# Kernel tuning notes

Measured on AMD Instinct MI355X. Metric: run time of the kernel, lower is better.

Reference implementation:

```python
import jax, jax.numpy as jnp
import numpy as np

NUM_HEADS = 8
CHUNK = 64          # dialtion / chunck_size
EPS = 1e-5          # InstanceNorm1d eps
NEG = -1e9


def setup_inputs() -> dict:
    key = jax.random.key(0)
    ks = jax.random.split(key, 8)
    N, C, T = 4, 512, 4096
    x = jax.random.normal(ks[0], (N, C, T), dtype=jnp.float32)
    q = jax.random.normal(ks[1], (N, C, T), dtype=jnp.float32)
    k = jax.random.normal(ks[2], (N, C, T), dtype=jnp.float32)
    v = jax.random.normal(ks[3], (N, C, T), dtype=jnp.float32)
    masks = jnp.ones((N, 1, T), dtype=jnp.float32)
    s = 1.0 / np.sqrt(C)
    W_in = jax.random.normal(ks[4], (3 * C, C), dtype=jnp.float32) * s   # packed q/k/v in-proj
    b_in = jnp.zeros((3 * C,), dtype=jnp.float32)
    W_out = jax.random.normal(ks[5], (C, C), dtype=jnp.float32) * s     # out-proj
    b_out = jnp.zeros((C,), dtype=jnp.float32)
    return {"x": x, "q": q, "k": k, "v": v, "masks": masks,
            "W_in": W_in, "b_in": b_in, "W_out": W_out, "b_out": b_out}


def _chunk_attn(q, k, v, masks, W_in, b_in, W_out, b_out):
    # q,k,v: [N, C, T]; masks: [N, 1, T]
    N, C, T = q.shape
    H, Dh = NUM_HEADS, C // NUM_HEADS
    nc = T // CHUNK
    Wq, Wk, Wv = jnp.split(W_in, 3, axis=0)
    bq, bk, bv = jnp.split(b_in, 3, axis=0)

    def proj(t, W, b):
        # [N,C,T] -> chunked heads [N, nc, CHUNK, H, Dh]
        t = t.transpose(0, 2, 1) @ W.T + b            # [N, T, C]
        return t.reshape(N, nc, CHUNK, H, Dh)

    qh = proj(q, Wq, bq)
    kh = proj(k, Wk, bk)
    vh = proj(v, Wv, bv)

    scale = 1.0 / jnp.sqrt(jnp.asarray(Dh, q.dtype))
    # intra-chunk scores: [N, nc, H, CHUNK, CHUNK]
    scores = jnp.einsum('bnqhd,bnkhd->bnhqk', qh, kh) * scale
    km = masks[:, 0, :].reshape(N, nc, CHUNK)         # key validity per chunk
    scores = scores + jnp.where(km[:, :, None, None, :] > 0, 0.0, NEG)
    attn = jax.nn.softmax(scores, axis=-1)
    out = jnp.einsum('bnhqk,bnkhd->bnqhd', attn, vh).reshape(N, T, C)
    out = out @ W_out.T + b_out                        # [N, T, C]
    out = out.transpose(0, 2, 1) * masks               # [N, C, T], re-mask
    return out


def reference(x, q, k, v, masks, W_in, b_in, W_out, b_out):
    out = _chunk_attn(q, k, v, masks, W_in, b_in, W_out, b_out) + x
    # InstanceNorm1d (affine=False): normalize each (n, c) row over T
    mu = jnp.mean(out, axis=2, keepdims=True)
    var = jnp.mean(jnp.square(out - mu), axis=2, keepdims=True)
    return (out - mu) * jax.lax.rsqrt(var + EPS)
```

## Files before the change

### kernel.cpp

```cpp
#include <hip/hip_runtime.h>
#include <hip/hip_bf16.h>

#define NB 4
#define CC 512
#define TT 4096
#define C3 1536
#define CQK 1024
#define NTC (NB*TT*CC)

typedef __attribute__((ext_vector_type(4))) float f32x4;
typedef __attribute__((ext_vector_type(8))) short short8;
typedef unsigned short ushort;
typedef __attribute__((ext_vector_type(8))) ushort u16x8;

__device__ __forceinline__ ushort f2bf(float f){
    union { float f; unsigned u; } x; x.f = f;
    unsigned r = x.u + 0x7fffu + ((x.u >> 16) & 1u);
    return (ushort)(r >> 16);
}

__device__ __forceinline__ ushort2 pk2bf(float a, float b){
    float2 f2; f2.x = a; f2.y = b;
    __hip_bfloat162 h = __float22bfloat162_rn(f2);
    union { __hip_bfloat162 h2; ushort2 u2; } u; u.h2 = h;
    return u.u2;
}

__device__ __forceinline__ void gload16(const void* g, void* l){
    __builtin_amdgcn_global_load_lds((const __attribute__((address_space(1))) void*)g,
                                     (__attribute__((address_space(3))) void*)l,
                                     16, 0, 0);
}

__device__ __forceinline__ int apos(int m, int cb){
    return (m*8 + ((cb + m + (m >> 3)) & 7))*8;
}

__global__ __launch_bounds__(256) void wcvt(const float* __restrict__ Wi,
                                            const float* __restrict__ Wo,
                                            ushort* __restrict__ Wb,
                                            ushort* __restrict__ Wob){
    int idx0 = blockIdx.x * 1024 + threadIdx.x;
    for (int i = 0; i < 4; ++i){
        int idx = idx0 + i*256;
        const float* src; ushort* dst; int j;
        if (idx < 196608){ src = Wi; dst = Wb;  j = idx; }
        else             { src = Wo; dst = Wob; j = idx - 196608; }
        f32x4 vv = *((const f32x4*)src + j);
        ushort4 o;
        *(ushort2*)&o.x = pk2bf(vv[0], vv[1]);
        *(ushort2*)&o.z = pk2bf(vv[2], vv[3]);
        *((ushort4*)dst + j) = o;
    }
}

__global__ __launch_bounds__(256, 3) void proj_gemm(const float* __restrict__ q,
                                                    const float* __restrict__ k,
                                                    const float* __restrict__ v,
                                                    const ushort* __restrict__ Wb,
                                                    const float* __restrict__ b_in,
                                                    ushort* __restrict__ P,
                                                    ushort* __restrict__ Vt){
    __shared__ __align__(16) ushort smem[24576];
    ushort* sA  = smem;
    ushort* sB0 = smem + 8192;
    ushort* sB1 = smem + 16384;
    const int tid = threadIdx.x;
    const int bid = blockIdx.x;
    const int l = (bid & 7)*192 + (bid >> 3);
    const int cotile = l % 12;
    const int mtile  = l / 12;
    const int co0 = cotile * 128;
    const int m0  = mtile * 128;
    const int which = co0 >> 9;
    const float* src = (which == 0) ? q : (which == 1) ? k : v;
    const int n  = m0 >> 12, t0 = m0 & 4095;
    const ushort* Bbase = Wb + (size_t)co0*CC;
    const int w = tid >> 6, lane = tid & 63;
    const int wr = w >> 1, wc = w & 1;
    const int l15 = lane & 15, quad = lane >> 4;
    const int hlf = lane >> 5, tq = lane & 31;

    const int mrB = tid >> 3;
    const int kkB = (tid & 7) ^ (mrB & 7);
    const ushort* gB0 = Bbase + (size_t)mrB*CC + kkB*8;
    const int lB0 = (tid & ~63) * 8;

    const float* Ab = src + (size_t)n*CC*TT + t0 + tq*4;
    const int ce0 = w*16 + hlf*2;

    f32x4 a0[4], a1[4];
    #pragma unroll
    for (int u = 0; u < 4; ++u){
        a0[u] = *(const f32x4*)(Ab + (size_t)(ce0 + u*4    )*TT);
        a1[u] = *(const f32x4*)(Ab + (size_t)(ce0 + u*4 + 1)*TT);
    }
    #pragma unroll
    for (int i = 0; i < 4; ++i)
        gload16(gB0 + (size_t)i*32*CC, sB0 + lB0 + i*2048);
    #pragma unroll
    for (int u = 0; u < 4; ++u){
        int ce = ce0 + u*4;
        int cb = ce >> 3, off = ce & 7;
        #pragma unroll
        for (int j = 0; j < 4; ++j)
            *(ushort2*)&sA[apos(tq*4 + j, cb) + off] = pk2bf(a0[u][j], a1[u][j]);
    }
    __syncthreads();

    f32x4 acc[4][4] = {};
    for (int kb = 0; kb < 8; ++kb){
        ushort* sBc = (kb & 1) ? sB1 : sB0;
        ushort* sBn = (kb & 1) ? sB0 : sB1;
        if (kb < 7){
            const float* Abn = Ab + (size_t)((kb+1)*64)*TT;
            #pragma unroll
            for (int u = 0; u < 4; ++u){
                a0[u] = *(const f32x4*)(Abn + (size_t)(ce0 + u*4    )*TT);
                a1[u] = *(const f32x4*)(Abn + (size_t)(ce0 + u*4 + 1)*TT);
            }
            #pragma unroll
            for (int i = 0; i < 4; ++i)
                gload16(gB0 + (size_t)i*32*CC + (kb+1)*64, sBn + lB0 + i*2048);
        }
        #pragma unroll
        for (int ks = 0; ks < 2; ++ks){
            short8 aF[4], bF[4];
            #pragma unroll
            for (int mi = 0; mi < 4; ++mi){
                int m = wr*64 + mi*16 + l15;
                aF[mi] = *(const short8*)&sA[apos(m, ks*4 + quad)];
            }
            #pragma unroll
            for (int ni = 0; ni < 4; ++ni){
                int m = wc*64 + ni*16 + l15;
                bF[ni] = *(const short8*)&sBc[(m*8 + ((ks*4 + quad) ^ (m & 7)))*8];
            }
            #pragma unroll
            for (int mi = 0; mi < 4; ++mi)
                #pragma unroll
                for (int ni = 0; ni < 4; ++ni)
                    acc[mi][ni] = __builtin_amdgcn_mfma_f32_16x16x32_bf16(
                        aF[mi], bF[ni], acc[mi][ni], 0, 0, 0);
        }
        __syncthreads();
        if (kb < 7){
            #pragma unroll
            for (int u = 0; u < 4; ++u){
                int ce = ce0 + u*4;
                int cb = ce >> 3, off = ce & 7;
                #pragma unroll
                for (int j = 0; j < 4; ++j)
                    *(ushort2*)&sA[apos(tq*4 + j, cb) + off] = pk2bf(a0[u][j], a1[u][j]);
            }
        }
        __syncthreads();
    }

    float bj[4];
    for (int ni = 0; ni < 4; ++ni) bj[ni] = b_in[co0 + wc*64 + ni*16 + l15];

    __syncthreads();
    ushort* sOut = smem;
    if (which < 2){
        for (int mi = 0; mi < 4; ++mi){
            int mrow = wr*64 + mi*16 + quad*4;
            for (int ni = 0; ni < 4; ++ni){
                int col = wc*64 + ni*16 + l15;
                for (int r = 0; r < 4; ++r)
                    sOut[(mrow + r)*136 + col] = f2bf(acc[mi][ni][r] + bj[ni]);
            }
        }
    } else {
        for (int mi = 0; mi < 4; ++mi){
            int mrow = wr*64 + mi*16 + quad*4;
            for (int ni = 0; ni < 4; ++ni){
                int col = wc*64 + ni*16 + l15;
                ushort4 o4;
                o4.x = f2bf(acc[mi][ni][0] + bj[ni]);
                o4.y = f2bf(acc[mi][ni][1] + bj[ni]);
                o4.z = f2bf(acc[mi][ni][2] + bj[ni]);
                o4.w = f2bf(acc[mi][ni][3] + bj[ni]);
                *(ushort4*)&sOut[col*136 + mrow] = o4;
            }
        }
    }
    __syncthreads();
    if (which < 2){
        for (int i = 0; i < 8; ++i){
            int flat = i*256 + tid;
            int row = flat >> 4, cs = (flat & 15)*8;
            u16x8 val = *(const u16x8*)&sOut[row*136 + cs];
            *(u16x8*)(P + (size_t)(m0 + row)*CQK + which*512 + (co0 & 511) + cs) = val;
        }
    } else {
        for (int i = 0; i < 8; ++i){
            int flat = i*256 + tid;
            int row = flat >> 4, cs = (flat & 15)*8;
            int cl = (co0 - 1024) + row;
            int h = cl >> 6, d = cl & 63;
            u16x8 val = *(const u16x8*)&sOut[row*136 + cs];
            *(u16x8*)(Vt + (((size_t)n*8 + h)*64 + d)*TT + t0 + cs) = val;
        }
    }
}

__global__ __launch_bounds__(256) void attn_kernel(const ushort* __restrict__ P,
                                                   const ushort* __restrict__ Vt,
                                                   const float* __restrict__ masks,
                                                   ushort* __restrict__ ctx){
    __shared__ __align__(16) ushort sQ[64*64], sK[64*64], sV[64*64];
    __shared__ __align__(16) ushort sP[64][72];
    __shared__ __align__(16) ushort sO[64*72];
    int bid = blockIdx.x;
    int l = (bid & 7)*256 + (bid >> 3);
    int h = l & 7, ch = (l >> 3) & 63, n = l >> 9;
    const int tid = threadIdx.x, lane = tid & 63, w = tid >> 6;
    const int l15 = lane & 15, quad = lane >> 4;
    const size_t rowbase = (size_t)n*TT + (size_t)ch*64;
    for (int i = 0; i < 2; ++i){
        int slot = i*256 + tid;
        int r = slot >> 3, k8 = slot & 7, kk = k8 ^ (r & 7);
        int lbase = (i*256 + (tid & ~63)) * 8;
        const ushort* gq = P + (rowbase + r)*CQK + h*64 + kk*8;
        gload16(gq,        sQ + lbase);
        gload16(gq + 512,  sK + lbase);
        const ushort* gv = Vt + (((size_t)n*8 + h)*64 + r)*TT + ch*64 + kk*8;
        gload16(gv,        sV + lbase);
    }
    __syncthreads();
    const int m0w = w*16;
    short8 aQ[2]; f32x4 accS[4] = {};
    for (int ks = 0; ks < 2; ++ks){
        int m = m0w + l15;
        aQ[ks] = *(const short8*)&sQ[(m*8 + ((ks*4 + quad) ^ (m & 7)))*8];
    }
    for (int ni = 0; ni < 4; ++ni)
        for (int ks = 0; ks < 2; ++ks){
            int m = ni*16 + l15;
            short8 bK = *(const short8*)&sK[(m*8 + ((ks*4 + quad) ^ (m & 7)))*8];
            accS[ni] = __builtin_amdgcn_mfma_f32_16x16x32_bf16(aQ[ks], bK, accS[ni], 0,0,0);
        }
    float madd[4];
    for (int ni = 0; ni < 4; ++ni){
        float mv = masks[(size_t)n*TT + ch*64 + ni*16 + l15];
        madd[ni] = (mv > 0.f) ? 0.f : -1e9f;
    }
    float s[4][4];
    for (int ni = 0; ni < 4; ++ni)
        for (int r = 0; r < 4; ++r) s[ni][r] = accS[ni][r]*0.125f + madd[ni];
    float ex[4][4];
    for (int r = 0; r < 4; ++r){
        float m1 = fmaxf(fmaxf(s[0][r], s[1][r]), fmaxf(s[2][r], s[3][r]));
        for (int d = 1; d < 16; d <<= 1) m1 = fmaxf(m1, __shfl_xor(m1, d));
        float a = 0.f;
        for (int ni = 0; ni < 4; ++ni){ float e = __expf(s[ni][r] - m1); ex[ni][r] = e; a += e; }
        for (int d = 1; d < 16; d <<= 1) a += __shfl_xor(a, d);
        float rs = 1.0f / a;
        for (int ni = 0; ni < 4; ++ni)
            sP[m0w + quad*4 + r][ni*16 + l15] = f2bf(ex[ni][r] * rs);
    }
    short8 aP[2]; f32x4 accO[4] = {};
    for (int ks = 0; ks < 2; ++ks)
        aP[ks] = *(const short8*)&sP[m0w + l15][ks*32 + quad*8];
    for (int ni = 0; ni < 4; ++ni)
        for (int ks = 0; ks < 2; ++ks){
            int m = ni*16 + l15;
            short8 bV = *(const short8*)&sV[(m*8 + ((ks*4 + quad) ^ (m & 7)))*8];
            accO[ni] = __builtin_amdgcn_mfma_f32_16x16x32_bf16(aP[ks], bV, accO[ni], 0,0,0);
        }
    for (int ni = 0; ni < 4; ++ni)
        for (int r = 0; r < 4; ++r)
            sO[(m0w + quad*4 + r)*72 + ni*16 + l15] = f2bf(accO[ni][r]);
    __syncthreads();
    for (int i = 0; i < 2; ++i){
        int flat = i*256 + tid;
        int row = flat >> 3, cs = (flat & 7)*8;
        u16x8 val = *(const u16x8*)&sO[row*72 + cs];
        *(u16x8*)(ctx + (rowbase + row)*CC + h*64 + cs) = val;
    }
}

__global__ __launch_bounds__(256) void out_gemm(const ushort* __restrict__ ctx,
                                                const ushort* __restrict__ Wob,
                                                const float* __restrict__ b_out,
                                                const float* __restrict__ x,
                                                const float* __restrict__ masks,
                                                float* __restrict__ out){
    __shared__ __align__(16) ushort smem[24576];
    ushort* sA0 = smem;
    ushort* sA1 = smem + 8192;
    ushort* sB0 = smem + 16384;
    ushort* sB1 = smem + 20480;
    float* fOut = (float*)smem;
    const int tid = threadIdx.x;
    const int bid = blockIdx.x;
    const int l = (bid & 7)*128 + (bid >> 3);
    const int cotile = l & 7;
    const int mtile  = l >> 3;
    const int co0 = cotile * 64;
    const int m0  = mtile * 128;
    const int n = m0 >> 12, t0 = m0 & 4095;
    const ushort* Abase = ctx + (size_t)m0*CC;
    const ushort* Bbase = Wob + (size_t)co0*CC;
    const int w = tid >> 6, lane = tid & 63;
    const int wr = w >> 1, wc = w & 1;
    const int l15 = lane & 15, quad = lane >> 4;

    const int mr = tid >> 3;
    const int kk = (tid & 7) ^ (mr & 7);
    const ushort* gA0 = Abase + (size_t)mr*CC + kk*8;
    const ushort* gB0 = Bbase + (size_t)mr*CC + kk*8;
    const int lS = (tid & ~63) * 8;

    #pragma unroll
    for (int i = 0; i < 4; ++i) gload16(gA0 + (size_t)i*32*CC, sA0 + lS + i*2048);
    #pragma unroll
    for (int i = 0; i < 2; ++i) gload16(gB0 + (size_t)i*32*CC, sB0 + lS + i*2048);

    f32x4 acc[4][2] = {};
    for (int kb = 0; kb < 8; ++kb){
        ushort* sAc = (kb & 1) ? sA1 : sA0;
        ushort* sBc = (kb & 1) ? sB1 : sB0;
        ushort* sAn = (kb & 1) ? sA0 : sA1;
        ushort* sBn = (kb & 1) ? sB0 : sB1;
        __syncthreads();
        if (kb < 7){
            #pragma unroll
            for (int i = 0; i < 4; ++i)
                gload16(gA0 + (size_t)i*32*CC + (kb+1)*64, sAn + lS + i*2048);
            #pragma unroll
            for (int i = 0; i < 2; ++i)
                gload16(gB0 + (size_t)i*32*CC + (kb+1)*64, sBn + lS + i*2048);
        }
        #pragma unroll
        for (int ks = 0; ks < 2; ++ks){
            short8 aF[4], bF[2];
            #pragma unroll
            for (int mi = 0; mi < 4; ++mi){
                int m = wr*64 + mi*16 + l15;
                aF[mi] = *(const short8*)&sAc[(m*8 + ((ks*4 + quad) ^ (m & 7)))*8];
            }
            #pragma unroll
            for (int ni = 0; ni < 2; ++ni){
                int m = wc*32 + ni*16 + l15;
                bF[ni] = *(const short8*)&sBc[(m*8 + ((ks*4 + quad) ^ (m & 7)))*8];
            }
            #pragma unroll
            for (int mi = 0; mi < 4; ++mi)
                #pragma unroll
                for (int ni = 0; ni < 2; ++ni)
                    acc[mi][ni] = __builtin_amdgcn_mfma_f32_16x16x32_bf16(
                        aF[mi], bF[ni], acc[mi][ni], 0, 0, 0);
        }
    }
    float bo[2];
    for (int ni = 0; ni < 2; ++ni) bo[ni] = b_out[co0 + wc*32 + ni*16 + l15];

    __syncthreads();
    for (int mi = 0; mi < 4; ++mi){
        int tl = wr*64 + mi*16 + quad*4;
        for (int ni = 0; ni < 2; ++ni){
            int cl = wc*32 + ni*16 + l15;
            f32x4 vv;
            for (int r = 0; r < 4; ++r) vv[r] = acc[mi][ni][r] + bo[ni];
            *(f32x4*)&fOut[cl*132 + tl] = vv;
        }
    }
    __syncthreads();
    for (int i = 0; i < 8; ++i){
        int flat = i*256 + tid;
        int co = flat >> 5, ts = (flat & 31)*4;
        f32x4 a = *(const f32x4*)&fOut[co*132 + ts];
        f32x4 mk = *(const f32x4*)(masks + (size_t)n*TT + t0 + ts);
        f32x4 xv = *(const f32x4*)(x + ((size_t)n*CC + co0 + co)*TT + t0 + ts);
        f32x4 o;
        for (int r = 0; r < 4; ++r) o[r] = a[r]*mk[r] + xv[r];
        *(f32x4*)(out + ((size_t)n*CC + co0 + co)*TT + t0 + ts) = o;
    }
}

__global__ __launch_bounds__(256) void inorm(float* __restrict__ out){
    __shared__ float sS[4], sQ2[4];
    float* row = out + (size_t)blockIdx.x * TT;
    f32x4 vbuf[4];
    float s = 0.f, ss = 0.f;
    for (int i = 0; i < 4; ++i){
        f32x4 vv = *(const f32x4*)(row + (size_t)(i*256 + threadIdx.x)*4);
        vbuf[i] = vv;
        for (int r = 0; r < 4; ++r){ s += vv[r]; ss += vv[r]*vv[r]; }
    }
    for (int d = 1; d < 64; d <<= 1){ s += __shfl_xor(s, d); ss += __shfl_xor(ss, d); }
    int w = threadIdx.x >> 6;
    if ((threadIdx.x & 63) == 0){ sS[w] = s; sQ2[w] = ss; }
    __syncthreads();
    s  = sS[0] + sS[1] + sS[2] + sS[3];
    ss = sQ2[0] + sQ2[1] + sQ2[2] + sQ2[3];
    float mean = s * (1.0f/TT);
    float var  = ss * (1.0f/TT) - mean*mean;
    float rstd = rsqrtf(var + 1e-5f);
    for (int i = 0; i < 4; ++i){
        f32x4 vv = vbuf[i], o;
        for (int r = 0; r < 4; ++r) o[r] = (vv[r] - mean) * rstd;
        *(f32x4*)(row + (size_t)(i*256 + threadIdx.x)*4) = o;
    }
}

extern "C" void kernel_launch(void* const* d_in, const int* in_sizes, int n_in,
                              void* d_out, int out_size, void* d_ws, size_t ws_size,
                              hipStream_t stream) {
    const float* x     = (const float*)d_in[0];
    const float* q     = (const float*)d_in[1];
    const float* k     = (const float*)d_in[2];
    const float* v     = (const float*)d_in[3];
    const float* masks = (const float*)d_in[4];
    const float* W_in  = (const float*)d_in[5];
    const float* b_in  = (const float*)d_in[6];
    const float* W_out = (const float*)d_in[7];
    const float* b_out = (const float*)d_in[8];
    float* out = (float*)d_out;

    ushort* ws  = (ushort*)d_ws;
    ushort* ctx = ws;
    ushort* Wb  = ws + (size_t)NTC;
    ushort* Wob = Wb + 786432;
    ushort* P   = Wob + 262144;
    ushort* Vt  = P + (size_t)NB*TT*CQK;

    wcvt<<<256, 256, 0, stream>>>(W_in, W_out, Wb, Wob);
    proj_gemm<<<1536, 256, 0, stream>>>(q, k, v, Wb, b_in, P, Vt);
    attn_kernel<<<2048, 256, 0, stream>>>(P, Vt, masks, ctx);
    out_gemm<<<1024, 256, 0, stream>>>(ctx, Wob, b_out, x, masks, out);
    inorm<<<2048, 256, 0, stream>>>(out);
}
```

Measured before the change: 242.2 us.

## Deepen software pipelining in projection and output GEMMs with explicit waitcnt barriers

The projection GEMM now prefetches A two K-blocks ahead using alternating register sets. It replaces __syncthreads with explicit vmcnt/lgkmcnt waits and sched barriers, and remaps the block index so co-tiles are outer. The output GEMM moves from double to triple LDS buffering with loads issued two stages ahead and counted waits. The aim is to hide global-load latency behind MFMA work, at the cost of more registers, more LDS (possibly lower occupancy) and fragile hand-written waitcnt logic. The projection kernel also drops its occupancy hint of 3 blocks.

Measured after the change: 238.9 us. No clear change (-1.3%).

```diff
diff --git a/kernel.cpp b/kernel.cpp
--- a/kernel.cpp
+++ b/kernel.cpp
@@ -12,6 +12,11 @@
 typedef __attribute__((ext_vector_type(8))) short short8;
 typedef unsigned short ushort;
 typedef __attribute__((ext_vector_type(8))) ushort u16x8;
+
+#define SBAR()  __builtin_amdgcn_s_barrier()
+#define SCHED0() __builtin_amdgcn_sched_barrier(0)
+#define WAITV(n) asm volatile("s_waitcnt vmcnt(" #n ")" ::: "memory")
+#define WAITLG() asm volatile("s_waitcnt lgkmcnt(0)" ::: "memory")
 
 __device__ __forceinline__ ushort f2bf(float f){
     union { float f; unsigned u; } x; x.f = f;
@@ -54,22 +59,21 @@
     }
 }
 
-__global__ __launch_bounds__(256, 3) void proj_gemm(const float* __restrict__ q,
-                                                    const float* __restrict__ k,
-                                                    const float* __restrict__ v,
-                                                    const ushort* __restrict__ Wb,
-                                                    const float* __restrict__ b_in,
-                                                    ushort* __restrict__ P,
-                                                    ushort* __restrict__ Vt){
+__global__ __launch_bounds__(256) void proj_gemm(const float* __restrict__ q,
+                                                 const float* __restrict__ k,
+                                                 const float* __restrict__ v,
+                                                 const ushort* __restrict__ Wb,
+                                                 const float* __restrict__ b_in,
+                                                 ushort* __restrict__ P,
+                                                 ushort* __restrict__ Vt){
     __shared__ __align__(16) ushort smem[24576];
     ushort* sA  = smem;
     ushort* sB0 = smem + 8192;
     ushort* sB1 = smem + 16384;
     const int tid = threadIdx.x;
     const int bid = blockIdx.x;
-    const int l = (bid & 7)*192 + (bid >> 3);
-    const int cotile = l % 12;
-    const int mtile  = l / 12;
+    const int mtile  = ((bid & 7) << 4) | ((bid >> 3) & 15);
+    const int cotile = bid >> 7;
     const int co0 = cotile * 128;
     const int m0  = mtile * 128;
     const int which = co0 >> 9;
@@ -89,73 +93,85 @@
     const float* Ab = src + (size_t)n*CC*TT + t0 + tq*4;
     const int ce0 = w*16 + hlf*2;
 
-    f32x4 a0[4], a1[4];
-    #pragma unroll
-    for (int u = 0; u < 4; ++u){
-        a0[u] = *(const f32x4*)(Ab + (size_t)(ce0 + u*4    )*TT);
-        a1[u] = *(const f32x4*)(Ab + (size_t)(ce0 + u*4 + 1)*TT);
-    }
-    #pragma unroll
-    for (int i = 0; i < 4; ++i)
-        gload16(gB0 + (size_t)i*32*CC, sB0 + lB0 + i*2048);
-    #pragma unroll
-    for (int u = 0; u < 4; ++u){
-        int ce = ce0 + u*4;
-        int cb = ce >> 3, off = ce & 7;
-        #pragma unroll
-        for (int j = 0; j < 4; ++j)
-            *(ushort2*)&sA[apos(tq*4 + j, cb) + off] = pk2bf(a0[u][j], a1[u][j]);
-    }
-    __syncthreads();
+    f32x4 aE[8], aO[8];
+
+#define LOADA(dst, cbase) do{                                              \
+    const float* _p = Ab + (size_t)(cbase)*TT;                             \
+    _Pragma("unroll")                                                      \
+    for (int u = 0; u < 4; ++u){                                           \
+        dst[2*u]   = *(const f32x4*)(_p + (size_t)(ce0 + u*4    )*TT);     \
+        dst[2*u+1] = *(const f32x4*)(_p + (size_t)(ce0 + u*4 + 1)*TT);     \
+    } }while(0)
+
+#define LOADB(buf, koff) do{                                               \
+    _Pragma("unroll")                                                      \
+    for (int i = 0; i < 4; ++i)                                            \
+        gload16(gB0 + (size_t)i*32*CC + (koff), (buf) + lB0 + i*2048);     \
+    }while(0)
+
+#define CVTA(sr) do{                                                       \
+    _Pragma("unroll")                                                      \
+    for (int u = 0; u < 4; ++u){                                           \
+        int ce = ce0 + u*4; int cb = ce >> 3, off = ce & 7;                \
+        _Pragma("unroll")                                                  \
+        for (int j = 0; j < 4; ++j)                                        \
+            *(ushort2*)&sA[apos(tq*4 + j, cb) + off] =                     \
+                pk2bf(sr[2*u][j], sr[2*u+1][j]);                           \
+    } }while(0)
+
+#define MFMAPH(sBc) do{                                                    \
+    _Pragma("unroll")                                                      \
+    for (int ks = 0; ks < 2; ++ks){                                        \
+        short8 aF[4], bF[4];                                               \
+        _Pragma("unroll")                                                  \
+        for (int mi = 0; mi < 4; ++mi){                                    \
+            int m = wr*64 + mi*16 + l15;                                   \
+            aF[mi] = *(const short8*)&sA[apos(m, ks*4 + quad)];            \
+        }                                                                  \
+        _Pragma("unroll")                                                  \
+        for (int ni = 0; ni < 4; ++ni){                                    \
+            int m = wc*64 + ni*16 + l15;                                   \
+            bF[ni] = *(const short8*)&(sBc)[(m*8 + ((ks*4 + quad) ^ (m & 7)))*8]; \
+        }                                                                  \
+        _Pragma("unroll")                                                  \
+        for (int mi = 0; mi < 4; ++mi)                                     \
+            _Pragma("unroll")                                              \
+            for (int ni = 0; ni < 4; ++ni)                                 \
+                acc[mi][ni] = __builtin_amdgcn_mfma_f32_16x16x32_bf16(     \
+                    aF[mi], bF[ni], acc[mi][ni], 0, 0, 0);                 \
+    } }while(0)
+
+#define PITER(kb, Lset, Cset, sBc, sBn) do{                                \
+    if ((kb) < 6) LOADA(Lset, ((kb)+2)*64);                                \
+    if ((kb) < 7) LOADB(sBn, ((kb)+1)*64);                                 \
+    SCHED0();                                                              \
+    if ((kb) < 6)      { WAITV(12); }                                      \
+    else if ((kb) == 6){ WAITV(4);  }                                      \
+    else               { WAITV(0);  }                                      \
+    WAITLG();                                                              \
+    SBAR();                       \
+    SCHED0();                                                              \
+    MFMAPH(sBc);                                                           \
+    SBAR();                  \
+    SCHED0();                                                              \
+    if ((kb) < 7) CVTA(Cset);                                              \
+    }while(0)
 
     f32x4 acc[4][4] = {};
-    for (int kb = 0; kb < 8; ++kb){
-        ushort* sBc = (kb & 1) ? sB1 : sB0;
-        ushort* sBn = (kb & 1) ? sB0 : sB1;
-        if (kb < 7){
-            const float* Abn = Ab + (size_t)((kb+1)*64)*TT;
-            #pragma unroll
-            for (int u = 0; u < 4; ++u){
-                a0[u] = *(const f32x4*)(Abn + (size_t)(ce0 + u*4    )*TT);
-                a1[u] = *(const f32x4*)(Abn + (size_t)(ce0 + u*4 + 1)*TT);
-            }
-            #pragma unroll
-            for (int i = 0; i < 4; ++i)
-                gload16(gB0 + (size_t)i*32*CC + (kb+1)*64, sBn + lB0 + i*2048);
-        }
-        #pragma unroll
-        for (int ks = 0; ks < 2; ++ks){
-            short8 aF[4], bF[4];
-            #pragma unroll
-            for (int mi = 0; mi < 4; ++mi){
-                int m = wr*64 + mi*16 + l15;
-                aF[mi] = *(const short8*)&sA[apos(m, ks*4 + quad)];
-            }
-            #pragma unroll
-            for (int ni = 0; ni < 4; ++ni){
-                int m = wc*64 + ni*16 + l15;
-                bF[ni] = *(const short8*)&sBc[(m*8 + ((ks*4 + quad) ^ (m & 7)))*8];
-            }
-            #pragma unroll
-            for (int mi = 0; mi < 4; ++mi)
-                #pragma unroll
-                for (int ni = 0; ni < 4; ++ni)
-                    acc[mi][ni] = __builtin_amdgcn_mfma_f32_16x16x32_bf16(
-                        aF[mi], bF[ni], acc[mi][ni], 0, 0, 0);
-        }
-        __syncthreads();
-        if (kb < 7){
-            #pragma unroll
-            for (int u = 0; u < 4; ++u){
-                int ce = ce0 + u*4;
-                int cb = ce >> 3, off = ce & 7;
-                #pragma unroll
-                for (int j = 0; j < 4; ++j)
-                    *(ushort2*)&sA[apos(tq*4 + j, cb) + off] = pk2bf(a0[u][j], a1[u][j]);
-            }
-        }
-        __syncthreads();
-    }
+    LOADA(aE, 0);
+    LOADB(sB0, 0);
+    LOADA(aO, 64);
+    CVTA(aE);
+    for (int kb2 = 0; kb2 < 8; kb2 += 2){
+        PITER(kb2,     aE, aO, sB0, sB1);
+        PITER(kb2 + 1, aO, aE, sB1, sB0);
+    }
+
+#undef LOADA
+#undef LOADB
+#undef CVTA
+#undef MFMAPH
+#undef PITER
 
     float bj[4];
     for (int ni = 0; ni < 4; ++ni) bj[ni] = b_in[co0 + wc*64 + ni*16 + l15];
@@ -287,11 +303,13 @@
                                                 const float* __restrict__ x,
                                                 const float* __restrict__ masks,
                                                 float* __restrict__ out){
-    __shared__ __align__(16) ushort smem[24576];
+    __shared__ __align__(16) ushort smem[36864];
     ushort* sA0 = smem;
     ushort* sA1 = smem + 8192;
-    ushort* sB0 = smem + 16384;
-    ushort* sB1 = smem + 20480;
+    ushort* sA2 = smem + 16384;
+    ushort* sB0 = smem + 24576;
+    ushort* sB1 = smem + 28672;
+    ushort* sB2 = smem + 32768;
     float* fOut = (float*)smem;
     const int tid = threadIdx.x;
     const int bid = blockIdx.x;
@@ -313,47 +331,57 @@
     const ushort* gB0 = Bbase + (size_t)mr*CC + kk*8;
     const int lS = (tid & ~63) * 8;
 
-    #pragma unroll
-    for (int i = 0; i < 4; ++i) gload16(gA0 + (size_t)i*32*CC, sA0 + lS + i*2048);
-    #pragma unroll
-    for (int i = 0; i < 2; ++i) gload16(gB0 + (size_t)i*32*CC, sB0 + lS + i*2048);
+#define OLOAD(sAn, sBn, koff) do{                                          \
+    _Pragma("unroll")                                                      \
+    for (int i = 0; i < 4; ++i)                                            \
+        gload16(gA0 + (size_t)i*32*CC + (koff), (sAn) + lS + i*2048);      \
+    _Pragma("unroll")                                                      \
+    for (int i = 0; i < 2; ++i)                                            \
+        gload16(gB0 + (size_t)i*32*CC + (koff), (sBn) + lS + i*2048);      \
+    }while(0)
+
+#define OITER(kb, sAc, sBc, sAn, sBn) do{                                  \
+    SCHED0();                                                              \
+    if ((kb) < 7) { WAITV(6); } else { WAITV(0); }                         \
+    SBAR();                                                                \
+    SCHED0();                                                              \
+    if ((kb) < 6) OLOAD(sAn, sBn, ((kb)+2)*64);                            \
+    _Pragma("unroll")                                                      \
+    for (int ks = 0; ks < 2; ++ks){                                        \
+        short8 aF[4], bF[2];                                               \
+        _Pragma("unroll")                                                  \
+        for (int mi = 0; mi < 4; ++mi){                                    \
+            int m = wr*64 + mi*16 + l15;                                   \
+            aF[mi] = *(const short8*)&(sAc)[(m*8 + ((ks*4 + quad) ^ (m & 7)))*8]; \
+        }                                                                  \
+        _Pragma("unroll")                                                  \
+        for (int ni = 0; ni < 2; ++ni){                                    \
+            int m = wc*32 + ni*16 + l15;                                   \
+            bF[ni] = *(const short8*)&(sBc)[(m*8 + ((ks*4 + quad) ^ (m & 7)))*8]; \
+        }                                                                  \
+        _Pragma("unroll")                                                  \
+        for (int mi = 0; mi < 4; ++mi)                                     \
+            _Pragma("unroll")                                              \
+            for (int ni = 0; ni < 2; ++ni)                                 \
+                acc[mi][ni] = __builtin_amdgcn_mfma_f32_16x16x32_bf16(     \
+                    aF[mi], bF[ni], acc[mi][ni], 0, 0, 0);                 \
+    } }while(0)
 
     f32x4 acc[4][2] = {};
-    for (int kb = 0; kb < 8; ++kb){
-        ushort* sAc = (kb & 1) ? sA1 : sA0;
-        ushort* sBc = (kb & 1) ? sB1 : sB0;
-        ushort* sAn = (kb & 1) ? sA0 : sA1;
-        ushort* sBn = (kb & 1) ? sB0 : sB1;
-        __syncthreads();
-        if (kb < 7){
-            #pragma unroll
-            for (int i = 0; i < 4; ++i)
-                gload16(gA0 + (size_t)i*32*CC + (kb+1)*64, sAn + lS + i*2048);
-            #pragma unroll
-            for (int i = 0; i < 2; ++i)
-                gload16(gB0 + (size_t)i*32*CC + (kb+1)*64, sBn + lS + i*2048);
-        }
-        #pragma unroll
-        for (int ks = 0; ks < 2; ++ks){
-            short8 aF[4], bF[2];
-            #pragma unroll
-            for (int mi = 0; mi < 4; ++mi){
-                int m = wr*64 + mi*16 + l15;
-                aF[mi] = *(const short8*)&sAc[(m*8 + ((ks*4 + quad) ^ (m & 7)))*8];
-            }
-            #pragma unroll
-            for (int ni = 0; ni < 2; ++ni){
-                int m = wc*32 + ni*16 + l15;
-                bF[ni] = *(const short8*)&sBc[(m*8 + ((ks*4 + quad) ^ (m & 7)))*8];
-            }
-            #pragma unroll
-            for (int mi = 0; mi < 4; ++mi)
-                #pragma unroll
-                for (int ni = 0; ni < 2; ++ni)
-                    acc[mi][ni] = __builtin_amdgcn_mfma_f32_16x16x32_bf16(
-                        aF[mi], bF[ni], acc[mi][ni], 0, 0, 0);
-        }
-    }
+    OLOAD(sA0, sB0, 0);
+    OLOAD(sA1, sB1, 64);
+    OITER(0, sA0, sB0, sA2, sB2);
+    OITER(1, sA1, sB1, sA0, sB0);
+    OITER(2, sA2, sB2, sA1, sB1);
+    OITER(3, sA0, sB0, sA2, sB2);
+    OITER(4, sA1, sB1, sA0, sB0);
+    OITER(5, sA2, sB2, sA1, sB1);
+    OITER(6, sA0, sB0, sA2, sB2);
+    OITER(7, sA1, sB1, sA0, sB0);
+
+#undef OLOAD
+#undef OITER
+
     float bo[2];
     for (int ni = 0; ni < 2; ++ni) bo[ni] = b_out[co0 + wc*32 + ni*16 + l15];
 
```
